# Performance work log

Hardware: AMD Instinct MI355X
Metric: run time of the kernel (lower is better)

Reference implementation:

```python
import jax, jax.numpy as jnp
import numpy as np

ALPHA = 0.2    # LeakyReLU negative slope (init arg alpha)
HEADS = 8
EPS = 1e-5     # LayerNorm eps


def setup_inputs() -> dict:
    key = jax.random.key(0)
    ks = jax.random.split(key, 16)
    B, S, D = 4, 1024, 256
    dh = D // HEADS  # 32
    x = jax.random.normal(ks[0], (B, S, D), jnp.float32)
    adj = (jax.random.uniform(ks[1], (B, S, S)) < 0.05).astype(jnp.float32)
    adj = jnp.maximum(adj, jnp.eye(S, dtype=jnp.float32)[None])

    def w(k, shape, fan):
        return jax.random.normal(k, shape, jnp.float32) * (fan ** -0.5)

    # GAT layer 0: in->hidden (concat heads)
    W0 = w(ks[2], (D, D), D); a_src0 = w(ks[3], (HEADS, dh), dh); a_dst0 = w(ks[4], (HEADS, dh), dh)
    # GAT layer 1: hidden->hidden (concat heads)
    W1 = w(ks[5], (D, D), D); a_src1 = w(ks[6], (HEADS, dh), dh); a_dst1 = w(ks[7], (HEADS, dh), dh)
    # GAT layer 2: hidden->out (mean over heads, head_dim = out_dim)
    W2 = w(ks[8], (D, HEADS * D), D); a_src2 = w(ks[9], (HEADS, D), D); a_dst2 = w(ks[10], (HEADS, D), D)
    # LayerNorm
    ln_g = jnp.ones((D,), jnp.float32); ln_b = jnp.zeros((D,), jnp.float32)
    # FFN: D -> 2D -> D
    ff_w1 = w(ks[11], (D, 2 * D), D); ff_b1 = jnp.zeros((2 * D,), jnp.float32)
    ff_w2 = w(ks[12], (2 * D, D), 2 * D); ff_b2 = jnp.zeros((D,), jnp.float32)
    return dict(adj=adj, x=x, W0=W0, a_src0=a_src0, a_dst0=a_dst0,
                W1=W1, a_src1=a_src1, a_dst1=a_dst1,
                W2=W2, a_src2=a_src2, a_dst2=a_dst2,
                ln_g=ln_g, ln_b=ln_b,
                ff_w1=ff_w1, ff_b1=ff_b1, ff_w2=ff_w2, ff_b2=ff_b2)


def _gat_layer(h, adj, W, a_src, a_dst, concat):
    B, S, _ = h.shape
    hp = jnp.einsum('bsi,io->bso', h, W).reshape(B, S, HEADS, -1)  # [B,S,H,dh]
    src = jnp.einsum('bshd,hd->bsh', hp, a_src)  # per-node source score
    dst = jnp.einsum('bshd,hd->bsh', hp, a_dst)  # per-node dest score
    # e[b,i,j,h] = LeakyReLU(src_i + dst_j), masked by adjacency
    e = jax.nn.leaky_relu(src[:, :, None, :] + dst[:, None, :, :], ALPHA)
    e = jnp.where(adj[..., None] > 0, e, jnp.float32(-1e9))
    attn = jax.nn.softmax(e, axis=2)  # softmax over neighbors j
    out = jnp.einsum('bijh,bjhd->bihd', attn, hp)
    return out.reshape(B, S, -1) if concat else out.mean(axis=2)


def reference(adj, x, W0, a_src0, a_dst0, W1, a_src1, a_dst1, W2, a_src2, a_dst2,
              ln_g, ln_b, ff_w1, ff_b1, ff_w2, ff_b2):
    # MultiAttentionGAT: 3 layers with residuals, ELU between layers
    h = jax.nn.elu(_gat_layer(x, adj, W0, a_src0, a_dst0, True) + x)
    h = jax.nn.elu(_gat_layer(h, adj, W1, a_src1, a_dst1, True) + h)
    h = _gat_layer(h, adj, W2, a_src2, a_dst2, False) + h
    # LayerNorm
    mu = h.mean(-1, keepdims=True)
    var = h.var(-1, keepdims=True)
    h = (h - mu) * jax.lax.rsqrt(var + EPS) * ln_g + ln_b
    # GELU FFN + residual
    ff = jnp.dot(jax.nn.gelu(jnp.dot(h, ff_w1) + ff_b1), ff_w2) + ff_b2
    return h + ff
```

## Files before the change

kernel.cpp:

```cpp
#include <hip/hip_runtime.h>
#include <hip/hip_bf16.h>

#define B_ 4
#define S_ 1024
#define D_ 256
#define H_ 8
#define LRELU_ALPHA 0.2f
#define MAXDEG 128

typedef __attribute__((ext_vector_type(8))) short short8;
typedef __attribute__((ext_vector_type(4))) float floatx4;

__device__ __forceinline__ float bf2f(unsigned short u) {
    union { unsigned int i; float f; } c; c.i = ((unsigned int)u) << 16; return c.f;
}
__device__ __forceinline__ unsigned short f2bf(float f) {
    union { float f; unsigned int u; } c; c.f = f;
    unsigned int r = (c.u + 0x7FFF + ((c.u >> 16) & 1)) >> 16;
    return (unsigned short)r;
}

__device__ void castT_body(const float* __restrict__ W, unsigned short* __restrict__ out,
                           int K, int N, int k0, int n0, float (*t)[33], int tid) {
    int tx = tid & 31, ty = tid >> 5;
#pragma unroll
    for (int i = 0; i < 4; ++i)
        t[ty + 8 * i][tx] = W[(size_t)(k0 + ty + 8 * i) * N + n0 + tx];
    __syncthreads();
#pragma unroll
    for (int i = 0; i < 4; ++i)
        out[(size_t)(n0 + ty + 8 * i) * K + k0 + tx] = f2bf(t[tx][ty + 8 * i]);
}

__global__ __launch_bounds__(256) void k_prep(
        const float* __restrict__ x, unsigned short* __restrict__ xb,
        const float* __restrict__ W0, unsigned short* __restrict__ W0t,
        const float* __restrict__ W1, unsigned short* __restrict__ W1t,
        const float* __restrict__ W2, unsigned short* __restrict__ W2t,
        const float* __restrict__ F1, unsigned short* __restrict__ F1t,
        const float* __restrict__ F2, unsigned short* __restrict__ F2t,
        const float* __restrict__ as2, const float* __restrict__ ad2,
        float* __restrict__ WS2, float* __restrict__ WD2,
        const float* __restrict__ adj, int* __restrict__ nbr, int* __restrict__ cnt) {
    __shared__ float t[32][33];
    __shared__ int c;
    int b = blockIdx.x, tid = threadIdx.x;
    if (b < 1024) {
        int i = b * 256 + tid;
        float4 v = ((const float4*)x)[i];
        ushort4 u; u.x = f2bf(v.x); u.y = f2bf(v.y); u.z = f2bf(v.z); u.w = f2bf(v.w);
        ((ushort4*)xb)[i] = u;
    } else if (b < 1088) {
        int i = b - 1024; castT_body(W0, W0t, 256, 256, (i & 7) * 32, (i >> 3) * 32, t, tid);
    } else if (b < 1152) {
        int i = b - 1088; castT_body(W1, W1t, 256, 256, (i & 7) * 32, (i >> 3) * 32, t, tid);
    } else if (b < 1664) {
        int i = b - 1152;
        int k0 = (i & 7) * 32, d0 = ((i >> 3) & 7) * 32, h = i >> 6;
        int tx = tid & 31, ty = tid >> 5;
#pragma unroll
        for (int q = 0; q < 4; ++q)
            t[ty + 8 * q][tx] = W2[(size_t)(k0 + ty + 8 * q) * 2048 + h * 256 + d0 + tx];
        __syncthreads();
#pragma unroll
        for (int q = 0; q < 4; ++q)
            W2t[(size_t)(d0 + ty + 8 * q) * 2048 + h * 256 + k0 + tx] = f2bf(t[tx][ty + 8 * q]);
    } else if (b < 1792) {
        int i = b - 1664; castT_body(F1, F1t, 256, 512, (i & 7) * 32, (i >> 3) * 32, t, tid);
    } else if (b < 1920) {
        int i = b - 1792; castT_body(F2, F2t, 512, 256, (i & 15) * 32, (i >> 4) * 32, t, tid);
    } else if (b < 1928) {
        int h = b - 1920, k = tid;
        const float* wrow = W2 + (size_t)k * 2048 + h * 256;
        float s = 0.f, d = 0.f;
        for (int dd = 0; dd < 256; ++dd) {
            float w = wrow[dd];
            s += w * as2[h * 256 + dd];
            d += w * ad2[h * 256 + dd];
        }
        WS2[h * 256 + k] = s;
        WD2[h * 256 + k] = d;
    } else {
        int row = b - 1928;
        if (tid == 0) c = 0;
        __syncthreads();
        float4 a4 = ((const float4*)(adj + (size_t)row * S_))[tid];
#pragma unroll
        for (int q = 0; q < 4; ++q) {
            float a = q == 0 ? a4.x : q == 1 ? a4.y : q == 2 ? a4.z : a4.w;
            if (a > 0.f) {
                int s = atomicAdd(&c, 1);
                if (s < MAXDEG) nbr[row * MAXDEG + s] = tid * 4 + q;
            }
        }
        __syncthreads();
        if (tid == 0) cnt[row] = c < MAXDEG ? c : MAXDEG;
    }
}

__global__ __launch_bounds__(256) void k_gemm_wide(const unsigned short* __restrict__ A,
        const unsigned short* __restrict__ Bt, float* __restrict__ P,
        int M, int N, int K, int Kc) {
    __shared__ unsigned short As[64][40];
    __shared__ unsigned short Bs[256][40];
    int tid = threadIdx.x;
    int bm = blockIdx.y * 64, bn = blockIdx.x * 256;
    int kbeg = blockIdx.z * Kc, kend = kbeg + Kc;
    int lane = tid & 63, wv = tid >> 6;
    int lrow = lane & 15, lq = lane >> 4;
    floatx4 acc[4][4] = {};
    int sm = tid >> 2, skq = (tid & 3) * 8;
    const unsigned short* Ap = A + (size_t)(bm + sm) * K + skq;
    const unsigned short* Bp0 = Bt + (size_t)(bn + sm) * K + skq;
    const unsigned short* Bp1 = Bp0 + (size_t)64 * K;
    const unsigned short* Bp2 = Bp0 + (size_t)128 * K;
    const unsigned short* Bp3 = Bp0 + (size_t)192 * K;
    short8 av  = *(const short8*)(Ap + kbeg);
    short8 bv0 = *(const short8*)(Bp0 + kbeg);
    short8 bv1 = *(const short8*)(Bp1 + kbeg);
    short8 bv2 = *(const short8*)(Bp2 + kbeg);
    short8 bv3 = *(const short8*)(Bp3 + kbeg);
    for (int k0 = kbeg; k0 < kend; k0 += 32) {
        *(short8*)&As[sm][skq]        = av;
        *(short8*)&Bs[sm][skq]        = bv0;
        *(short8*)&Bs[sm + 64][skq]   = bv1;
        *(short8*)&Bs[sm + 128][skq]  = bv2;
        *(short8*)&Bs[sm + 192][skq]  = bv3;
        __syncthreads();
        if (k0 + 32 < kend) {
            av  = *(const short8*)(Ap + k0 + 32);
            bv0 = *(const short8*)(Bp0 + k0 + 32);
            bv1 = *(const short8*)(Bp1 + k0 + 32);
            bv2 = *(const short8*)(Bp2 + k0 + 32);
            bv3 = *(const short8*)(Bp3 + k0 + 32);
        }
        short8 aF[4], bF[4];
#pragma unroll
        for (int mi = 0; mi < 4; ++mi)
            aF[mi] = *(const short8*)&As[mi * 16 + lrow][lq * 8];
#pragma unroll
        for (int ni = 0; ni < 4; ++ni)
            bF[ni] = *(const short8*)&Bs[wv * 64 + ni * 16 + lrow][lq * 8];
#pragma unroll
        for (int mi = 0; mi < 4; ++mi)
#pragma unroll
            for (int ni = 0; ni < 4; ++ni)
                acc[mi][ni] = __builtin_amdgcn_mfma_f32_16x16x32_bf16(aF[mi], bF[ni], acc[mi][ni], 0, 0, 0);
        __syncthreads();
    }
    float* out = P + (size_t)blockIdx.z * M * N;
#pragma unroll
    for (int mi = 0; mi < 4; ++mi)
#pragma unroll
        for (int ni = 0; ni < 4; ++ni)
#pragma unroll
            for (int r = 0; r < 4; ++r) {
                int grow = bm + mi * 16 + lq * 4 + r;
                int gcol = bn + wv * 64 + ni * 16 + lrow;
                out[(size_t)grow * N + gcol] = acc[mi][ni][r];
            }
}

__global__ __launch_bounds__(256) void k_red_scores(const float* __restrict__ P, int nsplit,
        const float* __restrict__ asrc, const float* __restrict__ adst,
        unsigned short* __restrict__ HPb, float* __restrict__ SRC, float* __restrict__ DST) {
    int row = blockIdx.x, tid = threadIdx.x;
    float v = P[(size_t)row * 256 + tid];
    for (int sp = 1; sp < nsplit; ++sp)
        v += P[(size_t)sp * 1048576 + (size_t)row * 256 + tid];
    HPb[(size_t)row * 256 + tid] = f2bf(v);
    float s = v * asrc[tid], d = v * adst[tid];
    for (int o = 16; o; o >>= 1) { s += __shfl_xor(s, o); d += __shfl_xor(d, o); }
    if ((tid & 31) == 0) {
        int h = tid >> 5;
        SRC[row * 8 + h] = s;
        DST[row * 8 + h] = d;
    }
}

__global__ __launch_bounds__(256) void k_attn_small_f(const unsigned short* __restrict__ hp,
        const float* __restrict__ src, const float* __restrict__ dst,
        const int* __restrict__ nbr, const int* __restrict__ cnts,
        const float* __restrict__ X, float* __restrict__ Hout,
        unsigned short* __restrict__ Hb,
        const float* __restrict__ WS2, const float* __restrict__ WD2,
        float* __restrict__ SRC2, float* __restrict__ DST2) {
    int tid = threadIdx.x;
    int half = tid >> 7;
    int sub = tid & 127;
    int row = blockIdx.x * 2 + half;
    int rb = row & ~(S_ - 1);
    __shared__ int nb[2][MAXDEG];
    __shared__ float ss[2][8];
    __shared__ float ew[2][MAXDEG * 9];
    __shared__ float pr[2][2][16];
    int cnt = cnts[row];
    for (int t = sub; t < cnt; t += 128) nb[half][t] = nbr[row * MAXDEG + t];
    if (sub < 8) ss[half][sub] = src[row * H_ + sub];
    __syncthreads();
    for (int idx = sub; idx < cnt * 8; idx += 128) {
        int n = idx >> 3, h = idx & 7;
        int j = nb[half][n];
        float e = ss[half][h] + dst[(rb + j) * H_ + h];
        ew[half][n * 9 + h] = e > 0.f ? e : LRELU_ALPHA * e;
    }
    __syncthreads();
    {
        int wv2 = sub >> 6, lane = sub & 63;
        int h = wv2 * 4 + (lane >> 4), s16 = lane & 15;
        float m = -1e30f;
        for (int n = s16; n < cnt; n += 16) m = fmaxf(m, ew[half][n * 9 + h]);
        for (int o = 8; o; o >>= 1) m = fmaxf(m, __shfl_xor(m, o));
        float s = 0.f;
        for (int n = s16; n < cnt; n += 16) {
            float v = __expf(ew[half][n * 9 + h] - m); ew[half][n * 9 + h] = v; s += v;
        }
        for (int o = 8; o; o >>= 1) s += __shfl_xor(s, o);
        float inv = s > 0.f ? 1.f / s : 0.f;
        for (int n = s16; n < cnt; n += 16) ew[half][n * 9 + h] *= inv;
    }
    __syncthreads();
    int d0 = sub * 2;
    int h = sub >> 4;
    const unsigned short* hpb = hp + (size_t)rb * 256 + d0;
    const float* ewr = ew[half];
    float aA0 = 0.f, aA1 = 0.f, aB0 = 0.f, aB1 = 0.f;
    float aC0 = 0.f, aC1 = 0.f, aD0 = 0.f, aD1 = 0.f;
    int n = 0;
    for (; n + 3 < cnt; n += 4) {
        int j0 = nb[half][n], j1 = nb[half][n + 1];
        int j2 = nb[half][n + 2], j3 = nb[half][n + 3];
        unsigned int p0 = *(const unsigned int*)(hpb + (size_t)j0 * 256);
        unsigned int p1 = *(const unsigned int*)(hpb + (size_t)j1 * 256);
        unsigned int p2 = *(const unsigned int*)(hpb + (size_t)j2 * 256);
        unsigned int p3 = *(const unsigned int*)(hpb + (size_t)j3 * 256);
        float w0 = ewr[n * 9 + h], w1 = ewr[(n + 1) * 9 + h];
        float w2 = ewr[(n + 2) * 9 + h], w3 = ewr[(n + 3) * 9 + h];
        aA0 += w0 * bf2f((unsigned short)p0); aA1 += w0 * bf2f((unsigned short)(p0 >> 16));
        aB0 += w1 * bf2f((unsigned short)p1); aB1 += w1 * bf2f((unsigned short)(p1 >> 16));
        aC0 += w2 * bf2f((unsigned short)p2); aC1 += w2 * bf2f((unsigned short)(p2 >> 16));
        aD0 += w3 * bf2f((unsigned short)p3); aD1 += w3 * bf2f((unsigned short)(p3 >> 16));
    }
    for (; n < cnt; ++n) {
        int j = nb[half][n];
        unsigned int p = *(const unsigned int*)(hpb + (size_t)j * 256);
        float w = ewr[n * 9 + h];
        aA0 += w * bf2f((unsigned short)p); aA1 += w * bf2f((unsigned short)(p >> 16));
    }
    float2 xv = *(const float2*)(X + (size_t)row * 256 + d0);
    float ov0 = (aA0 + aB0) + (aC0 + aD0) + xv.x;
    float ov1 = (aA1 + aB1) + (aC1 + aD1) + xv.y;
    ov0 = ov0 > 0.f ? ov0 : (__expf(ov0) - 1.f);
    ov1 = ov1 > 0.f ? ov1 : (__expf(ov1) - 1.f);
    *(float2*)(Hout + (size_t)row * 256 + d0) = make_float2(ov0, ov1);
    ushort2 ub; ub.x = f2bf(ov0); ub.y = f2bf(ov1);
    *(ushort2*)(Hb + (size_t)row * 256 + d0) = ub;
    if (WS2 != nullptr) {
        int wv2 = sub >> 6, lane = sub & 63;
#pragma unroll
        for (int hh = 0; hh < 8; ++hh) {
            float sP = ov0 * WS2[hh * 256 + d0] + ov1 * WS2[hh * 256 + d0 + 1];
            float dP = ov0 * WD2[hh * 256 + d0] + ov1 * WD2[hh * 256 + d0 + 1];
            for (int o = 32; o; o >>= 1) { sP += __shfl_xor(sP, o); dP += __shfl_xor(dP, o); }
            if (lane == 0) { pr[half][wv2][hh * 2] = sP; pr[half][wv2][hh * 2 + 1] = dP; }
        }
        __syncthreads();
        if (sub < 16) {
            float tv = pr[half][0][sub] + pr[half][1][sub];
            if ((sub & 1) == 0) SRC2[row * 8 + (sub >> 1)] = tv;
            else                DST2[row * 8 + (sub >> 1)] = tv;
        }
    }
}

__global__ __launch_bounds__(256) void k_attn_Y(const unsigned short* __restrict__ Hb,
        const float* __restrict__ src2, const float* __restrict__ dst2,
        const int* __restrict__ nbr, const int* __restrict__ cnts,
        unsigned short* __restrict__ Ycat) {
    int row = blockIdx.x;
    int tid = threadIdx.x;
    int rb = row & ~(S_ - 1);
    __shared__ int nb[MAXDEG];
    __shared__ float ss[8];
    __shared__ float ew[MAXDEG * 8];
    int cnt = cnts[row];
    for (int t = tid; t < cnt; t += 256) nb[t] = nbr[row * MAXDEG + t];
    if (tid < 8) ss[tid] = src2[row * H_ + tid];
    __syncthreads();
    for (int idx = tid; idx < cnt * 8; idx += 256) {
        int n = idx >> 3, h = idx & 7;
        int j = nb[n];
        float e = ss[h] + dst2[(rb + j) * H_ + h];
        ew[n * 8 + h] = e > 0.f ? e : LRELU_ALPHA * e;
    }
    __syncthreads();
    {
        int lane = tid & 63, wv = tid >> 6;
        int h = wv * 2 + (lane >> 5), sub = lane & 31;
        float m = -1e30f;
        for (int n = sub; n < cnt; n += 32) m = fmaxf(m, ew[n * 8 + h]);
        for (int o = 16; o; o >>= 1) m = fmaxf(m, __shfl_xor(m, o));
        float s = 0.f;
        for (int n = sub; n < cnt; n += 32) {
            float v = __expf(ew[n * 8 + h] - m); ew[n * 8 + h] = v; s += v;
        }
        for (int o = 16; o; o >>= 1) s += __shfl_xor(s, o);
        float inv = s > 0.f ? 0.125f / s : 0.f;
        for (int n = sub; n < cnt; n += 32) ew[n * 8 + h] *= inv;
    }
    __syncthreads();
    int dp = tid & 127, hg = tid >> 7;
    const unsigned short* hbase = Hb + (size_t)rb * 256 + 2 * dp;
    const float* ewh = ew + hg * 4;
    float a0x = 0.f, a0y = 0.f, a0z = 0.f, a0w = 0.f;
    float a1x = 0.f, a1y = 0.f, a1z = 0.f, a1w = 0.f;
    int n = 0;
    for (; n + 3 < cnt; n += 4) {
        int j0 = nb[n], j1 = nb[n + 1], j2 = nb[n + 2], j3 = nb[n + 3];
        unsigned int p0 = *(const unsigned int*)(hbase + (size_t)j0 * 256);
        unsigned int p1 = *(const unsigned int*)(hbase + (size_t)j1 * 256);
        unsigned int p2 = *(const unsigned int*)(hbase + (size_t)j2 * 256);
        unsigned int p3 = *(const unsigned int*)(hbase + (size_t)j3 * 256);
        float4 w0 = *(const float4*)(ewh + n * 8);
        float4 w1 = *(const float4*)(ewh + (n + 1) * 8);
        float4 w2 = *(const float4*)(ewh + (n + 2) * 8);
        float4 w3 = *(const float4*)(ewh + (n + 3) * 8);
        float v0a = bf2f((unsigned short)p0), v0b = bf2f((unsigned short)(p0 >> 16));
        float v1a = bf2f((unsigned short)p1), v1b = bf2f((unsigned short)(p1 >> 16));
        float v2a = bf2f((unsigned short)p2), v2b = bf2f((unsigned short)(p2 >> 16));
        float v3a = bf2f((unsigned short)p3), v3b = bf2f((unsigned short)(p3 >> 16));
        a0x += w0.x * v0a + w1.x * v1a + w2.x * v2a + w3.x * v3a;
        a0y += w0.y * v0a + w1.y * v1a + w2.y * v2a + w3.y * v3a;
        a0z += w0.z * v0a + w1.z * v1a + w2.z * v2a + w3.z * v3a;
        a0w += w0.w * v0a + w1.w * v1a + w2.w * v2a + w3.w * v3a;
        a1x += w0.x * v0b + w1.x * v1b + w2.x * v2b + w3.x * v3b;
        a1y += w0.y * v0b + w1.y * v1b + w2.y * v2b + w3.y * v3b;
        a1z += w0.z * v0b + w1.z * v1b + w2.z * v2b + w3.z * v3b;
        a1w += w0.w * v0b + w1.w * v1b + w2.w * v2b + w3.w * v3b;
    }
    for (; n < cnt; ++n) {
        int j = nb[n];
        unsigned int p = *(const unsigned int*)(hbase + (size_t)j * 256);
        float4 w = *(const float4*)(ewh + n * 8);
        float va = bf2f((unsigned short)p), vb = bf2f((unsigned short)(p >> 16));
        a0x += w.x * va; a0y += w.y * va; a0z += w.z * va; a0w += w.w * va;
        a1x += w.x * vb; a1y += w.y * vb; a1z += w.z * vb; a1w += w.w * vb;
    }
    unsigned short* yb = Ycat + (size_t)row * 2048 + (hg * 4) * 256 + 2 * dp;
    ushort2 u;
    u.x = f2bf(a0x); u.y = f2bf(a1x); *(ushort2*)(yb)         = u;
    u.x = f2bf(a0y); u.y = f2bf(a1y); *(ushort2*)(yb + 256)   = u;
    u.x = f2bf(a0z); u.y = f2bf(a1z); *(ushort2*)(yb + 512)   = u;
    u.x = f2bf(a0w); u.y = f2bf(a1w); *(ushort2*)(yb + 768)   = u;
}

__global__ __launch_bounds__(256) void k_ln_red(const float* __restrict__ P, int nsplit,
        const float* __restrict__ Hres, const float* __restrict__ g,
        const float* __restrict__ bta, float* __restrict__ HLN,
        unsigned short* __restrict__ HLNb) {
    int row = blockIdx.x * 4 + (threadIdx.x >> 6);
    int lane = threadIdx.x & 63;
    float4 v = ((const float4*)(Hres + (size_t)row * 256))[lane];
    for (int sp = 0; sp < nsplit; ++sp) {
        float4 p = ((const float4*)(P + (size_t)sp * 1048576 + (size_t)row * 256))[lane];
        v.x += p.x; v.y += p.y; v.z += p.z; v.w += p.w;
    }
    float s = v.x + v.y + v.z + v.w;
    float q = v.x * v.x + v.y * v.y + v.z * v.z + v.w * v.w;
    for (int o = 32; o; o >>= 1) { s += __shfl_xor(s, o); q += __shfl_xor(q, o); }
    float mu = s * (1.f / 256.f);
    float var = q * (1.f / 256.f) - mu * mu;
    if (var < 0.f) var = 0.f;
    float rs = rsqrtf(var + 1e-5f);
    float4 gg = ((const float4*)g)[lane];
    float4 bb = ((const float4*)bta)[lane];
    float4 o;
    o.x = (v.x - mu) * rs * gg.x + bb.x;
    o.y = (v.y - mu) * rs * gg.y + bb.y;
    o.z = (v.z - mu) * rs * gg.z + bb.z;
    o.w = (v.w - mu) * rs * gg.w + bb.w;
    ((float4*)(HLN + (size_t)row * 256))[lane] = o;
    ushort4 ob; ob.x = f2bf(o.x); ob.y = f2bf(o.y); ob.z = f2bf(o.z); ob.w = f2bf(o.w);
    ((ushort4*)(HLNb + (size_t)row * 256))[lane] = ob;
}

__global__ void k_red_gelu(const float* __restrict__ P, const float* __restrict__ b1,
                           unsigned short* __restrict__ out, int n, int nsplit, int cmask4) {
    int i = blockIdx.x * blockDim.x + threadIdx.x;
    if (i >= (n >> 2)) return;
    float4 s = ((const float4*)P)[i];
    for (int sp = 1; sp < nsplit; ++sp) {
        float4 v = ((const float4*)(P + (size_t)sp * n))[i];
        s.x += v.x; s.y += v.y; s.z += v.z; s.w += v.w;
    }
    float4 bb = ((const float4*)b1)[i & cmask4];
    float xs[4] = {s.x + bb.x, s.y + bb.y, s.z + bb.z, s.w + bb.w};
    ushort4 u;
    unsigned short* up = (unsigned short*)&u;
#pragma unroll
    for (int q = 0; q < 4; ++q) {
        float x = xs[q];
        float t = tanhf(0.7978845608028654f * (x + 0.044715f * x * x * x));
        up[q] = f2bf(0.5f * x * (1.f + t));
    }
    ((ushort4*)out)[i] = u;
}

__global__ void k_red_final(const float* __restrict__ P, const float* __restrict__ HLN,
                            const float* __restrict__ b2, float* __restrict__ out,
                            int n, int nsplit) {
    int i = blockIdx.x * blockDim.x + threadIdx.x;
    if (i >= (n >> 2)) return;
    float4 s = ((const float4*)HLN)[i];
    float4 bb = ((const float4*)b2)[i & 63];
    s.x += bb.x; s.y += bb.y; s.z += bb.z; s.w += bb.w;
    for (int sp = 0; sp < nsplit; ++sp) {
        float4 v = ((const float4*)(P + (size_t)sp * n))[i];
        s.x += v.x; s.y += v.y; s.z += v.z; s.w += v.w;
    }
    ((float4*)out)[i] = s;
}

extern "C" void kernel_launch(void* const* d_in, const int* in_sizes, int n_in,
                              void* d_out, int out_size, void* d_ws, size_t ws_size,
                              hipStream_t stream) {
    const float* adj   = (const float*)d_in[0];
    const float* x     = (const float*)d_in[1];
    const float* W0    = (const float*)d_in[2];
    const float* as0   = (const float*)d_in[3];
    const float* ad0   = (const float*)d_in[4];
    const float* W1    = (const float*)d_in[5];
    const float* as1   = (const float*)d_in[6];
    const float* ad1   = (const float*)d_in[7];
    const float* W2    = (const float*)d_in[8];
    const float* as2   = (const float*)d_in[9];
    const float* ad2   = (const float*)d_in[10];
    const float* ln_g  = (const float*)d_in[11];
    const float* ln_b  = (const float*)d_in[12];
    const float* ff_w1 = (const float*)d_in[13];
    const float* ff_b1 = (const float*)d_in[14];
    const float* ff_w2 = (const float*)d_in[15];
    const float* ff_b2 = (const float*)d_in[16];

    float* ws = (float*)d_ws;
    float* H    = ws;
    float* HLN  = ws + 1048576;
    unsigned short* Ycat = (unsigned short*)(ws + 2097152);
    unsigned short* HPb  = (unsigned short*)(ws + 6291456);
    unsigned short* xb   = (unsigned short*)(ws + 6815744);
    unsigned short* Hb   = (unsigned short*)(ws + 7340032);
    unsigned short* HLNb = (unsigned short*)(ws + 7864320);
    unsigned short* MIDb = (unsigned short*)(ws + 8388608);
    unsigned short* W0t  = (unsigned short*)(ws + 9437184);
    unsigned short* W1t  = (unsigned short*)(ws + 9469952);
    unsigned short* W2t  = (unsigned short*)(ws + 9502720);
    unsigned short* F1t  = (unsigned short*)(ws + 9764864);
    unsigned short* F2t  = (unsigned short*)(ws + 9830400);
    float* WS2  = ws + 9895936;
    float* WD2  = ws + 9897984;
    float* SRC  = ws + 9900032;
    float* DST  = ws + 9932800;
    float* SRC2 = ws + 9965568;
    float* DST2 = ws + 9998336;
    int*   NBR  = (int*)(ws + 10031104);
    int*   CNT  = (int*)(ws + 10555392);
    float* PP   = ws + 12582912;

    k_prep<<<6024, 256, 0, stream>>>(x, xb, W0, W0t, W1, W1t, W2, W2t,
                                     ff_w1, F1t, ff_w2, F2t, as2, ad2, WS2, WD2,
                                     adj, NBR, CNT);

    k_gemm_wide<<<dim3(1, 64, 4), 256, 0, stream>>>(xb, W0t, PP, 4096, 256, 256, 64);
    k_red_scores<<<4096, 256, 0, stream>>>(PP, 4, as0, ad0, HPb, SRC, DST);
    k_attn_small_f<<<2048, 256, 0, stream>>>(HPb, SRC, DST, NBR, CNT, x, H, Hb,
                                             nullptr, nullptr, nullptr, nullptr);

    k_gemm_wide<<<dim3(1, 64, 4), 256, 0, stream>>>(Hb, W1t, PP, 4096, 256, 256, 64);
    k_red_scores<<<4096, 256, 0, stream>>>(PP, 4, as1, ad1, HPb, SRC, DST);
    k_attn_small_f<<<2048, 256, 0, stream>>>(HPb, SRC, DST, NBR, CNT, H, H, Hb,
                                             WS2, WD2, SRC2, DST2);

    k_attn_Y<<<4096, 256, 0, stream>>>(Hb, SRC2, DST2, NBR, CNT, Ycat);
    k_gemm_wide<<<dim3(1, 64, 4), 256, 0, stream>>>(Ycat, W2t, PP, 4096, 256, 2048, 512);
    k_ln_red<<<1024, 256, 0, stream>>>(PP, 4, H, ln_g, ln_b, HLN, HLNb);

    k_gemm_wide<<<dim3(2, 64, 2), 256, 0, stream>>>(HLNb, F1t, PP, 4096, 512, 256, 128);
    k_red_gelu<<<2048, 256, 0, stream>>>(PP, ff_b1, MIDb, 2097152, 2, 127);
    k_gemm_wide<<<dim3(1, 64, 4), 256, 0, stream>>>(MIDb, F2t, PP, 4096, 256, 512, 128);
    k_red_final<<<1024, 256, 0, stream>>>(PP, HLN, ff_b2, (float*)d_out, 1048576, 4);
}
```

Baseline: 248.9 us.

## Replace split-K GEMMs with 64x64 tile GEMM and fused epilogues

Adds a 64x64-tile bf16 MFMA GEMM that keeps the full K reduction in one block and fuses the epilogue: bf16 output plus attention src/dst scores for the GAT layers, bias+GELU for FFN1, and bias+residual for FFN2. This drops four separate reduction kernels and the fp32 split-K partial buffer traffic they read and write. In exchange each block walks the whole K with a simple single-buffer loop, so per-block work grows and there is less parallelism along K.

Result: faster. 218.3 us (-12.3%).

```diff
diff --git a/kernel.cpp b/kernel.cpp
--- a/kernel.cpp
+++ b/kernel.cpp
@@ -161,20 +161,98 @@
             }
 }
 
-__global__ __launch_bounds__(256) void k_red_scores(const float* __restrict__ P, int nsplit,
-        const float* __restrict__ asrc, const float* __restrict__ adst,
-        unsigned short* __restrict__ HPb, float* __restrict__ SRC, float* __restrict__ DST) {
-    int row = blockIdx.x, tid = threadIdx.x;
-    float v = P[(size_t)row * 256 + tid];
-    for (int sp = 1; sp < nsplit; ++sp)
-        v += P[(size_t)sp * 1048576 + (size_t)row * 256 + tid];
-    HPb[(size_t)row * 256 + tid] = f2bf(v);
-    float s = v * asrc[tid], d = v * adst[tid];
-    for (int o = 16; o; o >>= 1) { s += __shfl_xor(s, o); d += __shfl_xor(d, o); }
-    if ((tid & 31) == 0) {
-        int h = tid >> 5;
-        SRC[row * 8 + h] = s;
-        DST[row * 8 + h] = d;
+template<int EPI>
+__global__ __launch_bounds__(256) void k_gemm64(
+        const unsigned short* __restrict__ A, const unsigned short* __restrict__ Bt,
+        int N, int K,
+        float* __restrict__ Pout, unsigned short* __restrict__ Ob,
+        const float* __restrict__ p1, const float* __restrict__ p2,
+        float* __restrict__ SRC, float* __restrict__ DST) {
+    __shared__ unsigned short As[64][40];
+    __shared__ unsigned short Bs[64][40];
+    int tid = threadIdx.x;
+    int bm = blockIdx.y * 64, bn = blockIdx.x * 64;
+    int lane = tid & 63, wv = tid >> 6;
+    int lrow = lane & 15, lq = lane >> 4;
+    floatx4 acc[4] = {};
+    int sm = tid >> 2, skq = (tid & 3) * 8;
+    const unsigned short* Ap = A + (size_t)(bm + sm) * K + skq;
+    const unsigned short* Bp = Bt + (size_t)(bn + sm) * K + skq;
+    short8 av = *(const short8*)Ap;
+    short8 bv = *(const short8*)Bp;
+    for (int k0 = 0; k0 < K; k0 += 32) {
+        *(short8*)&As[sm][skq] = av;
+        *(short8*)&Bs[sm][skq] = bv;
+        __syncthreads();
+        if (k0 + 32 < K) {
+            av = *(const short8*)(Ap + k0 + 32);
+            bv = *(const short8*)(Bp + k0 + 32);
+        }
+        short8 aF = *(const short8*)&As[wv * 16 + lrow][lq * 8];
+        short8 bF[4];
+#pragma unroll
+        for (int ni = 0; ni < 4; ++ni)
+            bF[ni] = *(const short8*)&Bs[ni * 16 + lrow][lq * 8];
+#pragma unroll
+        for (int ni = 0; ni < 4; ++ni)
+            acc[ni] = __builtin_amdgcn_mfma_f32_16x16x32_bf16(aF, bF[ni], acc[ni], 0, 0, 0);
+        __syncthreads();
+    }
+    int row0 = bm + wv * 16 + lq * 4;
+    if (EPI == 0) {
+#pragma unroll
+        for (int ni = 0; ni < 4; ++ni)
+#pragma unroll
+            for (int r = 0; r < 4; ++r)
+                Ob[(size_t)(row0 + r) * N + bn + ni * 16 + lrow] = f2bf(acc[ni][r]);
+        float asv[4], adv[4];
+#pragma unroll
+        for (int ni = 0; ni < 4; ++ni) {
+            asv[ni] = p1[bn + ni * 16 + lrow];
+            adv[ni] = p2[bn + ni * 16 + lrow];
+        }
+#pragma unroll
+        for (int r = 0; r < 4; ++r) {
+            float sA = acc[0][r] * asv[0] + acc[1][r] * asv[1];
+            float sB = acc[2][r] * asv[2] + acc[3][r] * asv[3];
+            float dA = acc[0][r] * adv[0] + acc[1][r] * adv[1];
+            float dB = acc[2][r] * adv[2] + acc[3][r] * adv[3];
+#pragma unroll
+            for (int o = 8; o; o >>= 1) {
+                sA += __shfl_xor(sA, o); sB += __shfl_xor(sB, o);
+                dA += __shfl_xor(dA, o); dB += __shfl_xor(dB, o);
+            }
+            if (lrow == 0) {
+                int h0 = bn >> 5;
+                SRC[(row0 + r) * 8 + h0]     = sA;
+                SRC[(row0 + r) * 8 + h0 + 1] = sB;
+                DST[(row0 + r) * 8 + h0]     = dA;
+                DST[(row0 + r) * 8 + h0 + 1] = dB;
+            }
+        }
+    } else if (EPI == 2) {
+#pragma unroll
+        for (int ni = 0; ni < 4; ++ni) {
+            int gcol = bn + ni * 16 + lrow;
+            float bb = p1[gcol];
+#pragma unroll
+            for (int r = 0; r < 4; ++r) {
+                float xx = acc[ni][r] + bb;
+                float tt = tanhf(0.7978845608028654f * (xx + 0.044715f * xx * xx * xx));
+                Ob[(size_t)(row0 + r) * N + gcol] = f2bf(0.5f * xx * (1.f + tt));
+            }
+        }
+    } else if (EPI == 3) {
+#pragma unroll
+        for (int ni = 0; ni < 4; ++ni) {
+            int gcol = bn + ni * 16 + lrow;
+            float bb = p1[gcol];
+#pragma unroll
+            for (int r = 0; r < 4; ++r) {
+                float res = p2[(size_t)(row0 + r) * 256 + gcol];
+                Pout[(size_t)(row0 + r) * 256 + gcol] = acc[ni][r] + bb + res;
+            }
+        }
     }
 }
 
@@ -384,43 +462,6 @@
     ((ushort4*)(HLNb + (size_t)row * 256))[lane] = ob;
 }
 
-__global__ void k_red_gelu(const float* __restrict__ P, const float* __restrict__ b1,
-                           unsigned short* __restrict__ out, int n, int nsplit, int cmask4) {
-    int i = blockIdx.x * blockDim.x + threadIdx.x;
-    if (i >= (n >> 2)) return;
-    float4 s = ((const float4*)P)[i];
-    for (int sp = 1; sp < nsplit; ++sp) {
-        float4 v = ((const float4*)(P + (size_t)sp * n))[i];
-        s.x += v.x; s.y += v.y; s.z += v.z; s.w += v.w;
-    }
-    float4 bb = ((const float4*)b1)[i & cmask4];
-    float xs[4] = {s.x + bb.x, s.y + bb.y, s.z + bb.z, s.w + bb.w};
-    ushort4 u;
-    unsigned short* up = (unsigned short*)&u;
-#pragma unroll
-    for (int q = 0; q < 4; ++q) {
-        float x = xs[q];
-        float t = tanhf(0.7978845608028654f * (x + 0.044715f * x * x * x));
-        up[q] = f2bf(0.5f * x * (1.f + t));
-    }
-    ((ushort4*)out)[i] = u;
-}
-
-__global__ void k_red_final(const float* __restrict__ P, const float* __restrict__ HLN,
-                            const float* __restrict__ b2, float* __restrict__ out,
-                            int n, int nsplit) {
-    int i = blockIdx.x * blockDim.x + threadIdx.x;
-    if (i >= (n >> 2)) return;
-    float4 s = ((const float4*)HLN)[i];
-    float4 bb = ((const float4*)b2)[i & 63];
-    s.x += bb.x; s.y += bb.y; s.z += bb.z; s.w += bb.w;
-    for (int sp = 0; sp < nsplit; ++sp) {
-        float4 v = ((const float4*)(P + (size_t)sp * n))[i];
-        s.x += v.x; s.y += v.y; s.z += v.z; s.w += v.w;
-    }
-    ((float4*)out)[i] = s;
-}
-
 extern "C" void kernel_launch(void* const* d_in, const int* in_sizes, int n_in,
                               void* d_out, int out_size, void* d_ws, size_t ws_size,
                               hipStream_t stream) {
@@ -470,13 +511,13 @@
                                      ff_w1, F1t, ff_w2, F2t, as2, ad2, WS2, WD2,
                                      adj, NBR, CNT);
 
-    k_gemm_wide<<<dim3(1, 64, 4), 256, 0, stream>>>(xb, W0t, PP, 4096, 256, 256, 64);
-    k_red_scores<<<4096, 256, 0, stream>>>(PP, 4, as0, ad0, HPb, SRC, DST);
+    k_gemm64<0><<<dim3(4, 64), 256, 0, stream>>>(xb, W0t, 256, 256,
+                                                 nullptr, HPb, as0, ad0, SRC, DST);
     k_attn_small_f<<<2048, 256, 0, stream>>>(HPb, SRC, DST, NBR, CNT, x, H, Hb,
                                              nullptr, nullptr, nullptr, nullptr);
 
-    k_gemm_wide<<<dim3(1, 64, 4), 256, 0, stream>>>(Hb, W1t, PP, 4096, 256, 256, 64);
-    k_red_scores<<<4096, 256, 0, stream>>>(PP, 4, as1, ad1, HPb, SRC, DST);
+    k_gemm64<0><<<dim3(4, 64), 256, 0, stream>>>(Hb, W1t, 256, 256,
+                                                 nullptr, HPb, as1, ad1, SRC, DST);
     k_attn_small_f<<<2048, 256, 0, stream>>>(HPb, SRC, DST, NBR, CNT, H, H, Hb,
                                              WS2, WD2, SRC2, DST2);
 
@@ -484,8 +525,8 @@
     k_gemm_wide<<<dim3(1, 64, 4), 256, 0, stream>>>(Ycat, W2t, PP, 4096, 256, 2048, 512);
     k_ln_red<<<1024, 256, 0, stream>>>(PP, 4, H, ln_g, ln_b, HLN, HLNb);
 
-    k_gemm_wide<<<dim3(2, 64, 2), 256, 0, stream>>>(HLNb, F1t, PP, 4096, 512, 256, 128);
-    k_red_gelu<<<2048, 256, 0, stream>>>(PP, ff_b1, MIDb, 2097152, 2, 127);
-    k_gemm_wide<<<dim3(1, 64, 4), 256, 0, stream>>>(MIDb, F2t, PP, 4096, 256, 512, 128);
-    k_red_final<<<1024, 256, 0, stream>>>(PP, HLN, ff_b2, (float*)d_out, 1048576, 4);
-}
+    k_gemm64<2><<<dim3(8, 64), 256, 0, stream>>>(HLNb, F1t, 512, 256,
+                                                 nullptr, MIDb, ff_b1, nullptr, nullptr, nullptr);
+    k_gemm64<3><<<dim3(4, 64), 256, 0, stream>>>(MIDb, F2t, 256, 512,
+                                                 (float*)d_out, nullptr, ff_b2, HLN, nullptr, nullptr);
+}
```
